# Optimization experiments

Measured on AMD Instinct MI355X. Metric: run time of the kernel, lower is better.

## Reference

```python
import jax, jax.numpy as jnp
import numpy as np

B, S, D = 4, 2048, 1024
H, HD = 16, 64
TAU = HD ** -0.5
N_MASKED = 256  # last keys masked (padding)


def setup_inputs() -> dict:
    key = jax.random.key(0)
    ks = jax.random.split(key, 8)
    sc = 0.02
    mask = jnp.zeros((B, 1, 1, S), dtype=bool).at[..., S - N_MASKED:].set(True)
    return {
        "q": jax.random.normal(ks[0], (B, S, D), dtype=jnp.float32),
        "k": jax.random.normal(ks[1], (B, S, D), dtype=jnp.float32),
        "v": jax.random.normal(ks[2], (B, S, D), dtype=jnp.float32),
        "mask": mask,
        "Wq": jax.random.normal(ks[3], (D, H * HD), dtype=jnp.float32) * sc,
        "bq": jnp.zeros((H * HD,), dtype=jnp.float32),
        "Wk": jax.random.normal(ks[4], (D, H * HD), dtype=jnp.float32) * sc,
        "bk": jnp.zeros((H * HD,), dtype=jnp.float32),
        "Wv": jax.random.normal(ks[5], (D, H * HD), dtype=jnp.float32) * sc,
        "bv": jnp.zeros((H * HD,), dtype=jnp.float32),
        "Wo": jax.random.normal(ks[6], (H * HD, D), dtype=jnp.float32) * sc,
        "bo": jnp.zeros((D,), dtype=jnp.float32),
    }


def reference(q, k, v, mask, Wq, bq, Wk, bk, Wv, bv, Wo, bo):
    # projections: [..., s, D] -> [..., s, H, HD]
    qh = (q @ Wq + bq).reshape(*q.shape[:-1], H, HD)
    kh = (k @ Wk + bk).reshape(*k.shape[:-1], H, HD)
    vh = (v @ Wv + bv).reshape(*v.shape[:-1], H, HD)
    # scores: [B, H, Q, K]
    attn = jnp.einsum('bqhd,bkhd->bhqk', qh, kh) * TAU
    attn = jnp.where(mask, -jnp.inf, attn)  # masked_fill(mask, -inf)
    # dropout(p=0) before softmax is identity
    p = jax.nn.softmax(attn, axis=-1)
    out = jnp.einsum('bhqk,bkhd->bqhd', p, vh).reshape(*q.shape[:-1], H * HD)
    return out @ Wo + bo  # [B, S, D]
```

## Files before the change

kernel.cpp:

```cpp
#include <hip/hip_runtime.h>
#include <hip/hip_fp16.h>
#include <cstdint>
#include <cstddef>

#define B_  4
#define S_  2048
#define D_  1024
#define H_  16
#define HD_ 64
#define TAU_ 0.125f

typedef _Float16 f16;
typedef __attribute__((ext_vector_type(8)))  _Float16 f16x8;
typedef __attribute__((ext_vector_type(4)))  _Float16 f16x4;
typedef __attribute__((ext_vector_type(2)))  __fp16   fp16x2_b;
typedef __attribute__((ext_vector_type(4)))  float    f32x4;
typedef __attribute__((ext_vector_type(16))) float    f32x16;
typedef __attribute__((ext_vector_type(2)))  unsigned u32x2;

__device__ __forceinline__ void gload_lds16(const f16* g, f16* l) {
    __builtin_amdgcn_global_load_lds(
        (const __attribute__((address_space(1))) unsigned int*)g,
        (__attribute__((address_space(3)))       unsigned int*)l,
        16, 0, 0);
}

__device__ __forceinline__ unsigned pkh(float a, float b) {
    fp16x2_b h = __builtin_amdgcn_cvt_pkrtz(a, b);
    return __builtin_bit_cast(unsigned, h);
}

__device__ __forceinline__ float pair_max(float x) {
    unsigned xu = __builtin_bit_cast(unsigned, x);
    u32x2 r = __builtin_amdgcn_permlane32_swap(xu, xu, false, false);
    return fmaxf(__builtin_bit_cast(float, r[0]), __builtin_bit_cast(float, r[1]));
}
__device__ __forceinline__ float pair_sum(float x) {
    unsigned xu = __builtin_bit_cast(unsigned, x);
    u32x2 r = __builtin_amdgcn_permlane32_swap(xu, xu, false, false);
    return __builtin_bit_cast(float, r[0]) + __builtin_bit_cast(float, r[1]);
}

__global__ __launch_bounds__(256) void mask_norm_kernel(
    const unsigned char* __restrict__ mp, unsigned char* __restrict__ nm,
    float* __restrict__ mf)
{
    __shared__ int flags[3];
    const int tid = threadIdx.x;
    if (tid < 3) flags[tid] = 0;
    __syncthreads();
    int loc0 = 0, loc1 = 0, loc2 = 0;
    for (int i = 0; i < 32; ++i) {
        int off = tid * 32 + i;
        unsigned char v = mp[off];
        if (v) {
            int m = off & 3;
            if (m == 0) loc0 = 1;
            else if (m == 1) loc1 = 1;
            else loc2 = 1;
        }
    }
    if (loc0) atomicOr(&flags[0], 1);
    if (loc1) atomicOr(&flags[1], 1);
    if (loc2) atomicOr(&flags[2], 1);
    __syncthreads();
    const int mode = flags[1] ? 0 : (flags[2] ? 2 : (flags[0] ? 1 : 0));
    for (int i = 0; i < 32; ++i) {
        int idx = tid * 32 + i;
        unsigned char r;
        if (mode == 0)      r = mp[idx] ? 1 : 0;
        else if (mode == 1) r = ((const int*)mp)[idx] ? 1 : 0;
        else                r = (((const float*)mp)[idx] != 0.f) ? 1 : 0;
        nm[idx] = r;
        mf[idx] = r ? -1e30f : 0.f;
    }
}

__global__ __launch_bounds__(256) void wconv_kernel(
    const float* __restrict__ W0, const float* __restrict__ W1,
    const float* __restrict__ W2, const float* __restrict__ W3,
    f16* __restrict__ Wt)
{
    __shared__ float T[64][65];
    const int z = blockIdx.z;
    const float* W = (z == 0) ? W0 : (z == 1) ? W1 : (z == 2) ? W2 : W3;
    f16* out = Wt + (size_t)z * D_ * D_;
    const int n0 = blockIdx.x * 64, k0 = blockIdx.y * 64;
    const int tid = threadIdx.x;
    for (int j = 0; j < 4; ++j) {
        int idx = j * 256 + tid;
        int r = idx >> 4, c4 = idx & 15;
        float4 v = *(const float4*)&W[(size_t)(k0 + r) * D_ + n0 + c4 * 4];
        T[r][c4 * 4 + 0] = v.x; T[r][c4 * 4 + 1] = v.y;
        T[r][c4 * 4 + 2] = v.z; T[r][c4 * 4 + 3] = v.w;
    }
    __syncthreads();
    for (int j = 0; j < 16; ++j) {
        int idx = j * 256 + tid;
        int nl = idx >> 6, kl = idx & 63;
        out[(size_t)(n0 + nl) * D_ + k0 + kl] = (f16)T[kl][nl];
    }
}

template <bool A16, bool OUT16, bool VTRANS>
__device__ __forceinline__ void gemm_body(
    const void* __restrict__ Ap, const f16* __restrict__ Wt,
    const float* __restrict__ bias, void* __restrict__ Cp,
    int m0, int n0)
{
    __shared__ __align__(16) f16 Al[128 * 64];
    __shared__ __align__(16) f16 Bl[128 * 64];
    const int tid = threadIdx.x, lane = tid & 63, wid = tid >> 6;
    const int wm = (wid >> 1) * 64, wn = (wid & 1) * 64;
    const int g = lane >> 4, c = lane & 15;

    f32x4 acc[4][4] = {};

    for (int kt = 0; kt < 16; ++kt) {
        const int k0 = kt * 64;
        for (int i = 0; i < 4; ++i) {
            int ch  = wid * 4 + i;
            int row = ch * 8 + (lane >> 3);
            int ls  = (lane & 7) ^ (row & 7);
            gload_lds16(Wt + (size_t)(n0 + row) * 1024 + k0 + ls * 8,
                        Bl + ch * 512);
        }
        if (A16) {
            const f16* A = (const f16*)Ap;
            for (int i = 0; i < 4; ++i) {
                int ch  = wid * 4 + i;
                int row = ch * 8 + (lane >> 3);
                int ls  = (lane & 7) ^ (row & 7);
                gload_lds16(A + (size_t)(m0 + row) * 1024 + k0 + ls * 8,
                            Al + ch * 512);
            }
        } else {
            const float* A = (const float*)Ap;
            for (int j = 0; j < 8; ++j) {
                int idx = j * 256 + tid;
                int row = idx >> 4, c4 = idx & 15;
                float4 v = *(const float4*)&A[(size_t)(m0 + row) * 1024 + k0 + c4 * 4];
                f16x4 h;
                h[0] = (f16)v.x; h[1] = (f16)v.y; h[2] = (f16)v.z; h[3] = (f16)v.w;
                int ps = (c4 >> 1) ^ (row & 7);
                *(f16x4*)&Al[row * 64 + ps * 8 + (c4 & 1) * 4] = h;
            }
        }
        __syncthreads();
        for (int kc = 0; kc < 2; ++kc) {
            f16x8 af[4], bf[4];
            for (int mb = 0; mb < 4; ++mb) {
                int row = wm + mb * 16 + c;
                af[mb] = *(const f16x8*)&Al[row * 64 + ((kc * 4 + g) ^ (row & 7)) * 8];
            }
            for (int nb = 0; nb < 4; ++nb) {
                int row = wn + nb * 16 + c;
                bf[nb] = *(const f16x8*)&Bl[row * 64 + ((kc * 4 + g) ^ (row & 7)) * 8];
            }
            for (int mb = 0; mb < 4; ++mb)
                for (int nb = 0; nb < 4; ++nb)
                    acc[mb][nb] = __builtin_amdgcn_mfma_f32_16x16x32_f16(
                        af[mb], bf[nb], acc[mb][nb], 0, 0, 0);
        }
        __syncthreads();
    }
    for (int nb = 0; nb < 4; ++nb) {
        int n = n0 + wn + nb * 16 + c;
        float bv = bias[n];
        for (int mb = 0; mb < 4; ++mb)
            for (int r = 0; r < 4; ++r) {
                int m = m0 + wm + mb * 16 + g * 4 + r;
                float v = acc[mb][nb][r] + bv;
                if (VTRANS) {
                    ((f16*)Cp)[(((size_t)(m >> 11) * H_ + (n >> 6)) * HD_ + (n & 63)) * S_ + (m & 2047)] = (f16)v;
                } else if (OUT16) {
                    ((f16*)Cp)[(size_t)m * 1024 + n] = (f16)v;
                } else {
                    ((float*)Cp)[(size_t)m * 1024 + n] = v;
                }
            }
    }
}

__global__ __launch_bounds__(256) void gemm_qkv_kernel(
    const float* __restrict__ q, const float* __restrict__ k,
    const float* __restrict__ v, const f16* __restrict__ Wt,
    const float* __restrict__ bq, const float* __restrict__ bk,
    const float* __restrict__ bv, f16* __restrict__ outbase)
{
    const int z = blockIdx.z;
    const float* A  = (z == 0) ? q  : (z == 1) ? k  : v;
    const float* bi = (z == 0) ? bq : (z == 1) ? bk : bv;
    const f16*  W   = Wt + (size_t)z * D_ * D_;
    f16* out        = outbase + (size_t)z * S_ * B_ * D_;
    if (z == 2)
        gemm_body<false, true, true >(A, W, bi, out, blockIdx.x * 128, blockIdx.y * 128);
    else
        gemm_body<false, true, false>(A, W, bi, out, blockIdx.x * 128, blockIdx.y * 128);
}

__global__ __launch_bounds__(256) void gemm_out_kernel(
    const f16* __restrict__ Oh, const f16* __restrict__ WtO,
    const float* __restrict__ bo, float* __restrict__ out)
{
    gemm_body<true, false, false>(Oh, WtO, bo, out, blockIdx.x * 128, blockIdx.y * 128);
}

__global__ __launch_bounds__(256) void attn_kernel(
    const f16* __restrict__ qh, const f16* __restrict__ kh,
    const f16* __restrict__ vt, const unsigned char* __restrict__ maskp,
    const float* __restrict__ maskf, f16* __restrict__ Oh)
{
    __shared__ __align__(16) f16 Kl[64 * 64];
    __shared__ __align__(16) f16 VTl[64 * 64];
    const int tid = threadIdx.x, lane = tid & 63, wid = tid >> 6;
    const int ql = lane & 31, hi = lane >> 5;
    const int h = blockIdx.y, b = blockIdx.z;
    const int q0 = blockIdx.x * 128 + wid * 32;

    f16x8 qf[4];
    {
        const f16* qrow = qh + ((size_t)(b * S_ + q0 + ql) * H_ + h) * HD_;
        #pragma unroll
        for (int dc = 0; dc < 4; ++dc) {
            f16x8 tq = *(const f16x8*)&qrow[dc * 16 + hi * 8];
            qf[dc] = tq * (_Float16)TAU_;
        }
    }

    float m_ = -1e30f, l_ = 0.f;
    f32x16 accO[2] = {};
    const unsigned char* mrow = maskp + (size_t)b * S_;
    const float* mfrow = maskf + (size_t)b * S_;
    const size_t kbase  = (size_t)b * S_ * D_ + (size_t)h * HD_;
    const size_t vtbase = ((size_t)b * H_ + h) * (size_t)HD_ * S_;

    for (int t = 0; t < 32; ++t) {
        const int kv0 = t * 64;
        unsigned char mb = mrow[kv0 + lane];
        unsigned long long bal = __ballot(mb != 0);
        if (bal == ~0ull) continue;
        const bool anyMask = bal != 0;

        #pragma unroll
        for (int i = 0; i < 2; ++i) {
            int ch  = wid * 2 + i;
            int row = ch * 8 + (lane >> 3);
            int ls  = (lane & 7) ^ (row & 7);
            gload_lds16(kh + kbase + (size_t)(kv0 + row) * D_ + ls * 8,
                        Kl + ch * 512);
        }
        #pragma unroll
        for (int i = 0; i < 2; ++i) {
            int ch  = wid * 2 + i;
            int row = ch * 8 + (lane >> 3);
            int ls  = (lane & 7) ^ (row & 7);
            gload_lds16(vt + vtbase + (size_t)row * S_ + kv0 + ls * 8,
                        VTl + ch * 512);
        }
        __syncthreads();

        f32x16 sacc[2] = {};
        #pragma unroll
        for (int ks = 0; ks < 2; ++ks) {
            const int key = ks * 32 + ql;
            #pragma unroll
            for (int dc = 0; dc < 4; ++dc) {
                int slot = (dc * 2 + hi) ^ (key & 7);
                f16x8 kf = *(const f16x8*)&Kl[key * 64 + slot * 8];
                sacc[ks] = __builtin_amdgcn_mfma_f32_32x32x16_f16(
                    kf, qf[dc], sacc[ks], 0, 0, 0);
            }
        }
        if (anyMask) {
            #pragma unroll
            for (int ks = 0; ks < 2; ++ks)
                #pragma unroll
                for (int r = 0; r < 16; ++r) {
                    int key = kv0 + ks * 32 + (r & 3) + 8 * (r >> 2) + 4 * hi;
                    sacc[ks][r] += mfrow[key];
                }
        }
        float mx = sacc[0][0];
        #pragma unroll
        for (int ks = 0; ks < 2; ++ks)
            #pragma unroll
            for (int r = 0; r < 16; ++r) mx = fmaxf(mx, sacc[ks][r]);
        mx = pair_max(mx);
        const float mnew = fmaxf(m_, mx);
        const float alpha = __expf(m_ - mnew);
        m_ = mnew;
        float ts = 0.f;
        #pragma unroll
        for (int ks = 0; ks < 2; ++ks)
            #pragma unroll
            for (int r = 0; r < 16; ++r) {
                float p = __expf(sacc[ks][r] - mnew);
                sacc[ks][r] = p;
                ts += p;
            }
        ts = pair_sum(ts);
        l_ = l_ * alpha + ts;
        #pragma unroll
        for (int blk = 0; blk < 2; ++blk)
            #pragma unroll
            for (int r = 0; r < 16; ++r) accO[blk][r] *= alpha;

        #pragma unroll
        for (int ks = 0; ks < 2; ++ks) {
            unsigned Pq[4][2];
            #pragma unroll
            for (int j = 0; j < 4; ++j) {
                Pq[j][0] = pkh(sacc[ks][4 * j + 0], sacc[ks][4 * j + 1]);
                Pq[j][1] = pkh(sacc[ks][4 * j + 2], sacc[ks][4 * j + 3]);
            }
            #pragma unroll
            for (int kc = 0; kc < 2; ++kc) {
                union { f16x8 v; unsigned u[4]; } pf;
                u32x2 s0 = __builtin_amdgcn_permlane32_swap(Pq[2 * kc][0], Pq[2 * kc + 1][0], false, false);
                u32x2 s1 = __builtin_amdgcn_permlane32_swap(Pq[2 * kc][1], Pq[2 * kc + 1][1], false, false);
                pf.u[0] = s0[0]; pf.u[2] = s0[1];
                pf.u[1] = s1[0]; pf.u[3] = s1[1];
                #pragma unroll
                for (int blk = 0; blk < 2; ++blk) {
                    int hd = blk * 32 + ql;
                    int slot = (ks * 4 + kc * 2 + hi) ^ (hd & 7);
                    f16x8 vtf = *(const f16x8*)&VTl[hd * 64 + slot * 8];
                    accO[blk] = __builtin_amdgcn_mfma_f32_32x32x16_f16(
                        vtf, pf.v, accO[blk], 0, 0, 0);
                }
            }
        }
        __syncthreads();
    }
    const float invl = 1.f / l_;
    f16* orow = Oh + ((size_t)(b * S_ + q0 + ql) * H_ + h) * HD_;
    #pragma unroll
    for (int blk = 0; blk < 2; ++blk)
        #pragma unroll
        for (int j = 0; j < 4; ++j) {
            f16x4 o;
            #pragma unroll
            for (int tt = 0; tt < 4; ++tt)
                o[tt] = (f16)(accO[blk][4 * j + tt] * invl);
            *(f16x4*)&orow[blk * 32 + 4 * hi + 8 * j] = o;
        }
}

extern "C" void kernel_launch(void* const* d_in, const int* in_sizes, int n_in,
                              void* d_out, int out_size, void* d_ws, size_t ws_size,
                              hipStream_t stream)
{
    const float* q    = (const float*)d_in[0];
    const float* k    = (const float*)d_in[1];
    const float* v    = (const float*)d_in[2];
    const unsigned char* mask = (const unsigned char*)d_in[3];
    const float* Wq   = (const float*)d_in[4];
    const float* bq   = (const float*)d_in[5];
    const float* Wk   = (const float*)d_in[6];
    const float* bk   = (const float*)d_in[7];
    const float* Wv   = (const float*)d_in[8];
    const float* bv   = (const float*)d_in[9];
    const float* Wo   = (const float*)d_in[10];
    const float* bo   = (const float*)d_in[11];
    float* out        = (float*)d_out;

    char* ws = (char*)d_ws;
    f16* Wt  = (f16*)ws;
    f16* qh  = (f16*)(ws + 8388608);
    f16* khp = (f16*)(ws + 8388608 + 16777216);
    f16* vtp = (f16*)(ws + 8388608 + 2 * 16777216);
    f16* Ohp = (f16*)(ws + 8388608 + 3 * 16777216);
    unsigned char* nm = (unsigned char*)(ws + 8388608 + 4 * 16777216);
    float* mf = (float*)(ws + 8388608 + 4 * 16777216 + 8192);

    mask_norm_kernel<<<1, 256, 0, stream>>>(mask, nm, mf);
    wconv_kernel<<<dim3(16, 16, 4), 256, 0, stream>>>(Wq, Wk, Wv, Wo, Wt);
    gemm_qkv_kernel<<<dim3(64, 8, 3), 256, 0, stream>>>(q, k, v, Wt, bq, bk, bv, qh);
    attn_kernel<<<dim3(16, 16, 4), 256, 0, stream>>>(qh, khp, vtp, nm, mf, Ohp);
    gemm_out_kernel<<<dim3(64, 8), 256, 0, stream>>>(Ohp, Wt + (size_t)3 * D_ * D_, bo, out);
}
```

Baseline: 252.7 us.

## Double-buffer attention K/V tiles, fold scale into Q, use exp2 with lazy rescale

```diff
diff --git a/kernel.cpp b/kernel.cpp
--- a/kernel.cpp
+++ b/kernel.cpp
@@ -9,6 +9,7 @@
 #define H_  16
 #define HD_ 64
 #define TAU_ 0.125f
+#define QSCALE_ 0.18033688011112042f
 
 typedef _Float16 f16;
 typedef __attribute__((ext_vector_type(8)))  _Float16 f16x8;
@@ -28,6 +29,12 @@
 __device__ __forceinline__ unsigned pkh(float a, float b) {
     fp16x2_b h = __builtin_amdgcn_cvt_pkrtz(a, b);
     return __builtin_bit_cast(unsigned, h);
+}
+
+__device__ __forceinline__ float exp2_hw(float x) {
+    float r;
+    asm("v_exp_f32 %0, %1" : "=v"(r) : "v"(x));
+    return r;
 }
 
 __device__ __forceinline__ float pair_max(float x) {
@@ -106,7 +113,7 @@
 __device__ __forceinline__ void gemm_body(
     const void* __restrict__ Ap, const f16* __restrict__ Wt,
     const float* __restrict__ bias, void* __restrict__ Cp,
-    int m0, int n0)
+    int m0, int n0, float oscale)
 {
     __shared__ __align__(16) f16 Al[128 * 64];
     __shared__ __align__(16) f16 Bl[128 * 64];
@@ -170,7 +177,7 @@
         for (int mb = 0; mb < 4; ++mb)
             for (int r = 0; r < 4; ++r) {
                 int m = m0 + wm + mb * 16 + g * 4 + r;
-                float v = acc[mb][nb][r] + bv;
+                float v = (acc[mb][nb][r] + bv) * oscale;
                 if (VTRANS) {
                     ((f16*)Cp)[(((size_t)(m >> 11) * H_ + (n >> 6)) * HD_ + (n & 63)) * S_ + (m & 2047)] = (f16)v;
                 } else if (OUT16) {
@@ -194,16 +201,17 @@
     const f16*  W   = Wt + (size_t)z * D_ * D_;
     f16* out        = outbase + (size_t)z * S_ * B_ * D_;
     if (z == 2)
-        gemm_body<false, true, true >(A, W, bi, out, blockIdx.x * 128, blockIdx.y * 128);
+        gemm_body<false, true, true >(A, W, bi, out, blockIdx.x * 128, blockIdx.y * 128, 1.f);
     else
-        gemm_body<false, true, false>(A, W, bi, out, blockIdx.x * 128, blockIdx.y * 128);
+        gemm_body<false, true, false>(A, W, bi, out, blockIdx.x * 128, blockIdx.y * 128,
+                                      z == 0 ? QSCALE_ : 1.f);
 }
 
 __global__ __launch_bounds__(256) void gemm_out_kernel(
     const f16* __restrict__ Oh, const f16* __restrict__ WtO,
     const float* __restrict__ bo, float* __restrict__ out)
 {
-    gemm_body<true, false, false>(Oh, WtO, bo, out, blockIdx.x * 128, blockIdx.y * 128);
+    gemm_body<true, false, false>(Oh, WtO, bo, out, blockIdx.x * 128, blockIdx.y * 128, 1.f);
 }
 
 __global__ __launch_bounds__(256) void attn_kernel(
@@ -211,129 +219,146 @@
     const f16* __restrict__ vt, const unsigned char* __restrict__ maskp,
     const float* __restrict__ maskf, f16* __restrict__ Oh)
 {
-    __shared__ __align__(16) f16 Kl[64 * 64];
-    __shared__ __align__(16) f16 VTl[64 * 64];
+    __shared__ __align__(16) f16 Kl[2][64 * 64];
+    __shared__ __align__(16) f16 VTl[2][64 * 64];
     const int tid = threadIdx.x, lane = tid & 63, wid = tid >> 6;
     const int ql = lane & 31, hi = lane >> 5;
-    const int h = blockIdx.y, b = blockIdx.z;
-    const int q0 = blockIdx.x * 128 + wid * 32;
+    const int lg = ((blockIdx.x & 7) << 7) + (blockIdx.x >> 3);
+    const int h = (lg >> 4) & 15, b = lg >> 8;
+    const int q0 = (lg & 15) * 128 + wid * 32;
+
+    const unsigned char* mrow = maskp + (size_t)b * S_;
+    const float* mfrow = maskf + (size_t)b * S_;
+    const size_t kbase  = (size_t)b * S_ * D_ + (size_t)h * HD_;
+    const size_t vtbase = ((size_t)b * H_ + h) * (size_t)HD_ * S_;
+
+    unsigned live = 0, part = 0;
+    for (int t = 0; t < 32; ++t) {
+        unsigned long long bal = __ballot(mrow[t * 64 + lane] != 0);
+        if (bal != ~0ull) {
+            live |= 1u << t;
+            if (bal) part |= 1u << t;
+        }
+    }
 
     f16x8 qf[4];
     {
         const f16* qrow = qh + ((size_t)(b * S_ + q0 + ql) * H_ + h) * HD_;
         #pragma unroll
-        for (int dc = 0; dc < 4; ++dc) {
-            f16x8 tq = *(const f16x8*)&qrow[dc * 16 + hi * 8];
-            qf[dc] = tq * (_Float16)TAU_;
-        }
+        for (int dc = 0; dc < 4; ++dc)
+            qf[dc] = *(const f16x8*)&qrow[dc * 16 + hi * 8];
     }
 
     float m_ = -1e30f, l_ = 0.f;
     f32x16 accO[2] = {};
-    const unsigned char* mrow = maskp + (size_t)b * S_;
-    const float* mfrow = maskf + (size_t)b * S_;
-    const size_t kbase  = (size_t)b * S_ * D_ + (size_t)h * HD_;
-    const size_t vtbase = ((size_t)b * H_ + h) * (size_t)HD_ * S_;
-
-    for (int t = 0; t < 32; ++t) {
-        const int kv0 = t * 64;
-        unsigned char mb = mrow[kv0 + lane];
-        unsigned long long bal = __ballot(mb != 0);
-        if (bal == ~0ull) continue;
-        const bool anyMask = bal != 0;
-
+
+    auto stage = [&](int kv0, int bb) {
         #pragma unroll
         for (int i = 0; i < 2; ++i) {
             int ch  = wid * 2 + i;
             int row = ch * 8 + (lane >> 3);
             int ls  = (lane & 7) ^ (row & 7);
             gload_lds16(kh + kbase + (size_t)(kv0 + row) * D_ + ls * 8,
-                        Kl + ch * 512);
-        }
-        #pragma unroll
-        for (int i = 0; i < 2; ++i) {
-            int ch  = wid * 2 + i;
-            int row = ch * 8 + (lane >> 3);
-            int ls  = (lane & 7) ^ (row & 7);
+                        &Kl[bb][ch * 512]);
             gload_lds16(vt + vtbase + (size_t)row * S_ + kv0 + ls * 8,
-                        VTl + ch * 512);
-        }
+                        &VTl[bb][ch * 512]);
+        }
+    };
+
+    if (live) {
+        int t = __builtin_ctz(live);
+        stage(t * 64, 0);
         __syncthreads();
-
-        f32x16 sacc[2] = {};
-        #pragma unroll
-        for (int ks = 0; ks < 2; ++ks) {
-            const int key = ks * 32 + ql;
+        int cur = 0;
+        for (;;) {
+            unsigned rem = live & (0xFFFFFFFEu << t);
+            int tn = rem ? __builtin_ctz(rem) : 32;
+            if (tn < 32) stage(tn * 64, cur ^ 1);
+
+            const int kv0 = t * 64;
+            const f16* Kb = &Kl[cur][0];
+            const f16* Vb = &VTl[cur][0];
+
+            f32x16 sacc[2] = {};
             #pragma unroll
-            for (int dc = 0; dc < 4; ++dc) {
-                int slot = (dc * 2 + hi) ^ (key & 7);
-                f16x8 kf = *(const f16x8*)&Kl[key * 64 + slot * 8];
-                sacc[ks] = __builtin_amdgcn_mfma_f32_32x32x16_f16(
-                    kf, qf[dc], sacc[ks], 0, 0, 0);
-            }
-        }
-        if (anyMask) {
+            for (int ks = 0; ks < 2; ++ks) {
+                const int key = ks * 32 + ql;
+                #pragma unroll
+                for (int dc = 0; dc < 4; ++dc) {
+                    int slot = (dc * 2 + hi) ^ (key & 7);
+                    f16x8 kf = *(const f16x8*)&Kb[key * 64 + slot * 8];
+                    sacc[ks] = __builtin_amdgcn_mfma_f32_32x32x16_f16(
+                        kf, qf[dc], sacc[ks], 0, 0, 0);
+                }
+            }
+            if (part & (1u << t)) {
+                #pragma unroll
+                for (int ks = 0; ks < 2; ++ks)
+                    #pragma unroll
+                    for (int r = 0; r < 16; ++r) {
+                        int key = kv0 + ks * 32 + (r & 3) + 8 * (r >> 2) + 4 * hi;
+                        sacc[ks][r] += mfrow[key];
+                    }
+            }
+            float mx = sacc[0][0];
             #pragma unroll
             for (int ks = 0; ks < 2; ++ks)
                 #pragma unroll
+                for (int r = 0; r < 16; ++r) mx = fmaxf(mx, sacc[ks][r]);
+            mx = pair_max(mx);
+            if (__ballot(mx > m_ + 8.f)) {
+                float mnew = fmaxf(m_, mx);
+                float alpha = exp2_hw(m_ - mnew);
+                m_ = mnew;
+                l_ *= alpha;
+                #pragma unroll
+                for (int blk = 0; blk < 2; ++blk)
+                    #pragma unroll
+                    for (int r = 0; r < 16; ++r) accO[blk][r] *= alpha;
+            }
+            float ts = 0.f;
+            #pragma unroll
+            for (int ks = 0; ks < 2; ++ks)
+                #pragma unroll
                 for (int r = 0; r < 16; ++r) {
-                    int key = kv0 + ks * 32 + (r & 3) + 8 * (r >> 2) + 4 * hi;
-                    sacc[ks][r] += mfrow[key];
+                    float p = exp2_hw(sacc[ks][r] - m_);
+                    sacc[ks][r] = p;
+                    ts += p;
                 }
-        }
-        float mx = sacc[0][0];
-        #pragma unroll
-        for (int ks = 0; ks < 2; ++ks)
+            l_ += pair_sum(ts);
+
             #pragma unroll
-            for (int r = 0; r < 16; ++r) mx = fmaxf(mx, sacc[ks][r]);
-        mx = pair_max(mx);
-        const float mnew = fmaxf(m_, mx);
-        const float alpha = __expf(m_ - mnew);
-        m_ = mnew;
-        float ts = 0.f;
-        #pragma unroll
-        for (int ks = 0; ks < 2; ++ks)
-            #pragma unroll
-            for (int r = 0; r < 16; ++r) {
-                float p = __expf(sacc[ks][r] - mnew);
-                sacc[ks][r] = p;
-                ts += p;
-            }
-        ts = pair_sum(ts);
-        l_ = l_ * alpha + ts;
-        #pragma unroll
-        for (int blk = 0; blk < 2; ++blk)
-            #pragma unroll
-            for (int r = 0; r < 16; ++r) accO[blk][r] *= alpha;
-
-        #pragma unroll
-        for (int ks = 0; ks < 2; ++ks) {
-            unsigned Pq[4][2];
-            #pragma unroll
-            for (int j = 0; j < 4; ++j) {
-                Pq[j][0] = pkh(sacc[ks][4 * j + 0], sacc[ks][4 * j + 1]);
-                Pq[j][1] = pkh(sacc[ks][4 * j + 2], sacc[ks][4 * j + 3]);
-            }
-            #pragma unroll
-            for (int kc = 0; kc < 2; ++kc) {
-                union { f16x8 v; unsigned u[4]; } pf;
-                u32x2 s0 = __builtin_amdgcn_permlane32_swap(Pq[2 * kc][0], Pq[2 * kc + 1][0], false, false);
-                u32x2 s1 = __builtin_amdgcn_permlane32_swap(Pq[2 * kc][1], Pq[2 * kc + 1][1], false, false);
-                pf.u[0] = s0[0]; pf.u[2] = s0[1];
-                pf.u[1] = s1[0]; pf.u[3] = s1[1];
-                #pragma unroll
-                for (int blk = 0; blk < 2; ++blk) {
-                    int hd = blk * 32 + ql;
-                    int slot = (ks * 4 + kc * 2 + hi) ^ (hd & 7);
-                    f16x8 vtf = *(const f16x8*)&VTl[hd * 64 + slot * 8];
-                    accO[blk] = __builtin_amdgcn_mfma_f32_32x32x16_f16(
-                        vtf, pf.v, accO[blk], 0, 0, 0);
+            for (int ks = 0; ks < 2; ++ks) {
+                unsigned Pq[4][2];
+                #pragma unroll
+                for (int j = 0; j < 4; ++j) {
+                    Pq[j][0] = pkh(sacc[ks][4 * j + 0], sacc[ks][4 * j + 1]);
+                    Pq[j][1] = pkh(sacc[ks][4 * j + 2], sacc[ks][4 * j + 3]);
                 }
-            }
-        }
-        __syncthreads();
-    }
-    const float invl = 1.f / l_;
+                #pragma unroll
+                for (int kc = 0; kc < 2; ++kc) {
+                    union { f16x8 v; unsigned u[4]; } pf;
+                    u32x2 s0 = __builtin_amdgcn_permlane32_swap(Pq[2 * kc][0], Pq[2 * kc + 1][0], false, false);
+                    u32x2 s1 = __builtin_amdgcn_permlane32_swap(Pq[2 * kc][1], Pq[2 * kc + 1][1], false, false);
+                    pf.u[0] = s0[0]; pf.u[2] = s0[1];
+                    pf.u[1] = s1[0]; pf.u[3] = s1[1];
+                    #pragma unroll
+                    for (int blk = 0; blk < 2; ++blk) {
+                        int hd = blk * 32 + ql;
+                        int slot = (ks * 4 + kc * 2 + hi) ^ (hd & 7);
+                        f16x8 vtf = *(const f16x8*)&Vb[hd * 64 + slot * 8];
+                        accO[blk] = __builtin_amdgcn_mfma_f32_32x32x16_f16(
+                            vtf, pf.v, accO[blk], 0, 0, 0);
+                    }
+                }
+            }
+            __syncthreads();
+            cur ^= 1;
+            if (tn == 32) break;
+            t = tn;
+        }
+    }
+    const float invl = (l_ > 0.f) ? 1.f / l_ : 0.f;
     f16* orow = Oh + ((size_t)(b * S_ + q0 + ql) * H_ + h) * HD_;
     #pragma unroll
     for (int blk = 0; blk < 2; ++blk)
@@ -377,6 +402,6 @@
     mask_norm_kernel<<<1, 256, 0, stream>>>(mask, nm, mf);
     wconv_kernel<<<dim3(16, 16, 4), 256, 0, stream>>>(Wq, Wk, Wv, Wo, Wt);
     gemm_qkv_kernel<<<dim3(64, 8, 3), 256, 0, stream>>>(q, k, v, Wt, bq, bk, bv, qh);
-    attn_kernel<<<dim3(16, 16, 4), 256, 0, stream>>>(qh, khp, vtp, nm, mf, Ohp);
+    attn_kernel<<<1024, 256, 0, stream>>>(qh, khp, vtp, nm, mf, Ohp);
     gemm_out_kernel<<<dim3(64, 8), 256, 0, stream>>>(Ohp, Wt + (size_t)3 * D_ * D_, bo, out);
 }
```

After: 248.5 us. About the same (-1.7%).
